# Kernel optimization log

Hardware: AMD Instinct MI355X
Metric: run time of the kernel (lower is better)

The kernel has to match this reference:

```python
import jax, jax.numpy as jnp
import numpy as np

B, L, E, H = 4, 2048, 512, 8


def setup_inputs() -> dict:
    key = jax.random.key(0)
    ks = jax.random.split(key, 12)
    s = 0.02
    inp = {
        "values": jax.random.normal(ks[0], (B, L, E), jnp.float32),
        "keys": jax.random.normal(ks[1], (B, L, E), jnp.float32),
        "queries": jax.random.normal(ks[2], (B, L, E), jnp.float32),
    }
    mask = jax.random.randint(ks[3], (B, L, H, H), 0, 2, jnp.int32)
    # guarantee at least one unmasked entry per softmax row to avoid NaN rows
    mask = mask.at[..., 0].set(1)
    inp["mask"] = mask
    # Linear(E, E*H) weights stored as (in, out); torch uses y = x @ W.T + b
    inp["Wv"] = jax.random.normal(ks[4], (E, E * H), jnp.float32) * s
    inp["bv"] = jnp.zeros((E * H,), jnp.float32)
    inp["Wk"] = jax.random.normal(ks[5], (E, E * H), jnp.float32) * s
    inp["bk"] = jnp.zeros((E * H,), jnp.float32)
    inp["Wq"] = jax.random.normal(ks[6], (E, E * H), jnp.float32) * s
    inp["bq"] = jnp.zeros((E * H,), jnp.float32)
    inp["Wo"] = jax.random.normal(ks[7], (E * H, E), jnp.float32) * s
    inp["bo"] = jnp.zeros((E,), jnp.float32)
    return inp


def reference(values, keys, queries, mask, Wv, bv, Wk, bk, Wq, bq, Wo, bo):
    b, l, e = queries.shape
    h = Wq.shape[1] // e

    def proj(x, W, bias):
        # (B,L,E) -> (B,L,H,E) -> transpose(1,2) -> (B,H,L,E)
        return (x @ W + bias).reshape(b, -1, h, e).transpose(0, 2, 1, 3)

    v = proj(values, Wv, bv)
    k = proj(keys, Wk, bk)
    q = proj(queries, Wq, bq)
    # Faithful to source: einsum labels applied to the TRANSPOSED (B,H,L,E)
    # tensors, so 'q'/'k' bind to the heads axis and 'h' binds to seq axis.
    # energy: (B, L, H, H) -- head-vs-head scores at each position.
    energy = jnp.einsum('nqhd,nkhd->nhqk', q, k)
    energy = jnp.where(mask == 0, -jnp.inf, energy)
    attn = jax.nn.softmax(energy / jnp.sqrt(jnp.float32(e)), axis=3)
    # out of einsum: (B, H, L, E); raw row-major reshape to (B, L, H*E)
    out = jnp.einsum('nhql,nlhd->nqhd', attn, v).reshape(b, -1, h * e)
    return out @ Wo + bo
```

## Files before the change

### kernel.cpp

```cpp
#include <hip/hip_runtime.h>
#include <stdint.h>

typedef __attribute__((ext_vector_type(4))) float f32x4;
typedef __attribute__((ext_vector_type(8))) __bf16 bf16x8;

__device__ __forceinline__ unsigned short f2bf(float f) {
  union { float f; uint32_t u; } v; v.f = f;
  uint32_t u = v.u;
  return (unsigned short)((u + 0x7FFFu + ((u >> 16) & 1u)) >> 16);
}
__device__ __forceinline__ float bflo(uint32_t u) {
  union { uint32_t u; float f; } v; v.u = u << 16; return v.f;
}
__device__ __forceinline__ float bfhi(uint32_t u) {
  union { uint32_t u; float f; } v; v.u = u & 0xffff0000u; return v.f;
}

__device__ __forceinline__ void async_copy16(void* lds, const void* g) {
  __builtin_amdgcn_global_load_lds(
      (const __attribute__((address_space(1))) void*)g,
      (__attribute__((address_space(3))) void*)lds,
      16, 0, 0);
}

__global__ void cvt3_f32_bf16(const float* __restrict__ in0,
                              const float* __restrict__ in1,
                              const float* __restrict__ in2,
                              uint32_t* __restrict__ out, int n) {
  const float* in = (blockIdx.y == 0) ? in0 : (blockIdx.y == 1) ? in1 : in2;
  uint32_t* o = out + (size_t)blockIdx.y * (n / 2);
  int i = blockIdx.x * blockDim.x + threadIdx.x;
  int idx = i * 8;
  if (idx >= n) return;
  float4 a = *(const float4*)(in + idx);
  float4 b = *(const float4*)(in + idx + 4);
  uint4 ov;
  ov.x = f2bf(a.x) | ((uint32_t)f2bf(a.y) << 16);
  ov.y = f2bf(a.z) | ((uint32_t)f2bf(a.w) << 16);
  ov.z = f2bf(b.x) | ((uint32_t)f2bf(b.y) << 16);
  ov.w = f2bf(b.z) | ((uint32_t)f2bf(b.w) << 16);
  *(uint4*)(o + i * 4) = ov;
}

__global__ void transpose3_to_bf16(const float* __restrict__ in0,
                                   const float* __restrict__ in1,
                                   const float* __restrict__ in2,
                                   unsigned short* __restrict__ out,
                                   int R, int C) {
  const float* in = (blockIdx.z == 0) ? in0 : (blockIdx.z == 1) ? in1 : in2;
  unsigned short* o = out + (size_t)blockIdx.z * ((size_t)R * C);
  __shared__ float tile[32][33];
  int c0 = blockIdx.x * 32, r0 = blockIdx.y * 32;
  int tx = threadIdx.x, ty = threadIdx.y;
  #pragma unroll
  for (int rr = 0; rr < 32; rr += 8)
    tile[ty + rr][tx] = in[(size_t)(r0 + ty + rr) * C + c0 + tx];
  __syncthreads();
  #pragma unroll
  for (int rr = 0; rr < 32; rr += 8)
    o[(size_t)(c0 + ty + rr) * R + r0 + tx] = f2bf(tile[tx][ty + rr]);
}

__global__ void transpose_to_bf16(const float* __restrict__ in,
                                  unsigned short* __restrict__ out,
                                  int R, int C) {
  __shared__ float tile[32][33];
  int c0 = blockIdx.x * 32, r0 = blockIdx.y * 32;
  int tx = threadIdx.x, ty = threadIdx.y;
  #pragma unroll
  for (int rr = 0; rr < 32; rr += 8)
    tile[ty + rr][tx] = in[(size_t)(r0 + ty + rr) * C + c0 + tx];
  __syncthreads();
  #pragma unroll
  for (int rr = 0; rr < 32; rr += 8)
    out[(size_t)(c0 + ty + rr) * R + r0 + tx] = f2bf(tile[tx][ty + rr]);
}

template <int NK, int NN, bool PARTIAL>
__global__ __launch_bounds__(512, 2) void gemm256(
    const unsigned short* __restrict__ A,
    const unsigned short* __restrict__ Bt,
    const float* __restrict__ bias,
    void* __restrict__ Cout,
    int Mt, int NtG, int KC, int Kfull) {
  constexpr int TT = NK * NN;
  static_assert(TT >= 4 && (TT % 2) == 0, "need even TT >= 4");
  __shared__ unsigned short lds[2 * 2 * 256 * 64];

  const int nwg = Mt * NtG * KC;
  const int cpx = nwg >> 3;
  const int bid = blockIdx.x;
  const int nb = (bid & 7) * cpx + (bid >> 3);
  const int kc = nb / (Mt * NtG);
  const int r2 = nb % (Mt * NtG);
  const int bm = r2 / NtG;
  const int ng = r2 % NtG;
  const int N = NtG * NN * 256;
  const size_t koff = (size_t)kc * (NK * 64);

  const int tid = threadIdx.x;
  const int wv = tid >> 6, ln = tid & 63;
  const int wm = wv >> 2, wn = wv & 3;

  f32x4 acc[8][4] = {};
  bf16x8 af[4][2];
  bf16x8 bfb[2][2];

  char* const lds0 = (char*)lds;
  char* const lds1 = (char*)lds + 65536;

  auto stage_A = [&](int h, int tau, char* dstbuf) {
    const int kt = tau % NK;
    #pragma unroll
    for (int r = 0; r < 2; ++r) {
      const int rb = r * 128 + h * 64 + wv * 8;
      const int row = rb + (ln >> 3);
      const int kcs = (ln & 7) ^ (row & 7);
      const unsigned short* g =
          A + (size_t)(bm * 256 + row) * Kfull + koff + kt * 64 + kcs * 8;
      async_copy16(dstbuf + rb * 128, g);
    }
  };
  auto stage_B = [&](int h, int tau, char* dstbuf) {
    const int kt = tau % NK;
    const int bnn = ng * NN + tau / NK;
    #pragma unroll
    for (int r = 0; r < 2; ++r) {
      const int s = r * 2 + (wv >> 2);
      const int rb = s * 64 + h * 32 + (wv & 3) * 8;
      const int row = rb + (ln >> 3);
      const int kcs = (ln & 7) ^ (row & 7);
      const unsigned short* g =
          Bt + (size_t)(bnn * 256 + row) * Kfull + koff + kt * 64 + kcs * 8;
      async_copy16(dstbuf + 32768 + rb * 128, g);
    }
  };
  auto load_af = [&](int mh, const char* buf) {
    #pragma unroll
    for (int f = 0; f < 4; ++f) {
      const int lr = wm * 128 + (mh * 4 + f) * 16 + (ln & 15);
      #pragma unroll
      for (int s = 0; s < 2; ++s) {
        const int kq = s * 4 + (ln >> 4);
        af[f][s] = *(const bf16x8*)(buf + lr * 128 + ((kq ^ (lr & 7)) * 16));
      }
    }
  };
  auto load_bf = [&](int nh, const char* buf) {
    #pragma unroll
    for (int gq = 0; gq < 2; ++gq) {
      const int lr = wn * 64 + (nh * 2 + gq) * 16 + (ln & 15);
      #pragma unroll
      for (int s = 0; s < 2; ++s) {
        const int kq = s * 4 + (ln >> 4);
        bfb[gq][s] =
            *(const bf16x8*)(buf + 32768 + lr * 128 + ((kq ^ (lr & 7)) * 16));
      }
    }
  };
  auto mfma_quad = [&](int mh, int nh) {
    __builtin_amdgcn_sched_barrier(0);
    __builtin_amdgcn_s_barrier();
    __builtin_amdgcn_sched_barrier(0);
    __builtin_amdgcn_s_setprio(1);
    #pragma unroll
    for (int f = 0; f < 4; ++f)
      #pragma unroll
      for (int gq = 0; gq < 2; ++gq)
        #pragma unroll
        for (int s = 0; s < 2; ++s)
          acc[mh * 4 + f][nh * 2 + gq] = __builtin_amdgcn_mfma_f32_16x16x32_bf16(
              bfb[gq][s], af[f][s], acc[mh * 4 + f][nh * 2 + gq], 0, 0, 0);
    __builtin_amdgcn_s_setprio(0);
    __builtin_amdgcn_sched_barrier(0);
  };
  auto epilogue = [&](int nt) {
    const int m0 = bm * 256 + wm * 128 + (ln & 15);
    const int n0 = (ng * NN + nt) * 256 + wn * 64 + ((ln >> 4) << 2);
    if (PARTIAL) {
      float* Cp = (float*)Cout + (size_t)kc * ((size_t)Mt * 256) * N;
      #pragma unroll
      for (int f = 0; f < 8; ++f) {
        const int row = m0 + f * 16;
        #pragma unroll
        for (int g = 0; g < 4; ++g)
          *(f32x4*)(Cp + (size_t)row * N + n0 + g * 16) = acc[f][g];
      }
    } else {
      unsigned short* C = (unsigned short*)Cout;
      #pragma unroll
      for (int f = 0; f < 8; ++f) {
        const int row = m0 + f * 16;
        #pragma unroll
        for (int g = 0; g < 4; ++g) {
          const int col = n0 + g * 16;
          float4 bv = *(const float4*)(bias + col);
          uint2 o;
          o.x = f2bf(acc[f][g][0] + bv.x) | ((uint32_t)f2bf(acc[f][g][1] + bv.y) << 16);
          o.y = f2bf(acc[f][g][2] + bv.z) | ((uint32_t)f2bf(acc[f][g][3] + bv.w) << 16);
          *(uint2*)(C + (size_t)row * N + col) = o;
        }
      }
    }
    #pragma unroll
    for (int f = 0; f < 8; ++f)
      #pragma unroll
      for (int g = 0; g < 4; ++g)
        acc[f][g] = (f32x4){0.f, 0.f, 0.f, 0.f};
  };

  auto tile_body = [&](int tau, char* buf, char* obuf) {
    load_af(0, buf); load_bf(0, buf);
    if (tau + 1 < TT) stage_B(0, tau + 1, obuf);
    mfma_quad(0, 0);
    __builtin_amdgcn_s_barrier();
    load_bf(1, buf);
    if (tau + 2 < TT) stage_A(0, tau + 2, buf);
    mfma_quad(0, 1);
    __builtin_amdgcn_s_barrier();
    load_af(1, buf);
    if (tau + 2 < TT) stage_B(1, tau + 2, buf);
    mfma_quad(1, 1);
    __builtin_amdgcn_s_barrier();
    load_bf(0, buf);
    if (tau + 2 < TT) stage_A(1, tau + 2, buf);
    mfma_quad(1, 0);
    if (tau + 2 < TT) {
      asm volatile("s_waitcnt vmcnt(6)" ::: "memory");
    } else if (tau + 1 < TT) {
      asm volatile("s_waitcnt vmcnt(0)" ::: "memory");
    }
    __builtin_amdgcn_sched_barrier(0);
    __builtin_amdgcn_s_barrier();
    if ((tau + 1) % NK == 0) epilogue(tau / NK);
  };

  stage_A(0, 0, lds0); stage_B(1, 0, lds0); stage_A(1, 0, lds0); stage_B(0, 0, lds0);
  stage_A(0, 1, lds1); stage_B(1, 1, lds1); stage_A(1, 1, lds1);
  asm volatile("s_waitcnt vmcnt(6)" ::: "memory");
  __builtin_amdgcn_sched_barrier(0);
  __builtin_amdgcn_s_barrier();

  for (int it = 0; it < TT / 2; ++it) {
    tile_body(2 * it,     lds0, lds1);
    tile_body(2 * it + 1, lds1, lds0);
  }
}

__global__ void reduce4_bias(const float* __restrict__ p,
                             const float* __restrict__ bo,
                             float* __restrict__ out) {
  const size_t S = (size_t)8192 * 512;
  size_t i = ((size_t)blockIdx.x * 256 + threadIdx.x) * 4;
  float4 a = *(const float4*)(p + i);
  float4 b = *(const float4*)(p + S + i);
  float4 c = *(const float4*)(p + 2 * S + i);
  float4 d = *(const float4*)(p + 3 * S + i);
  float4 bb = *(const float4*)(bo + (int)(i & 511));
  float4 o;
  o.x = a.x + b.x + c.x + d.x + bb.x;
  o.y = a.y + b.y + c.y + d.y + bb.y;
  o.z = a.z + b.z + c.z + d.z + bb.z;
  o.w = a.w + b.w + c.w + d.w + bb.w;
  *(float4*)(out + i) = o;
}

__global__ __launch_bounds__(256) void energy_mfma(
    const unsigned short* __restrict__ Q,
    const unsigned short* __restrict__ Kb,
    const int* __restrict__ mask,
    float* __restrict__ P) {
  const int wave = threadIdx.x >> 6, ln = threadIdx.x & 63;
  const int t2 = (blockIdx.x * 4 + wave) * 2;
  const int r16 = ln & 15;
  const int g = ln >> 4;
  const size_t rowoff = (size_t)(t2 + (r16 >> 3)) * 4096 + (r16 & 7) * 512 + g * 8;
  const unsigned short* qb = Q + rowoff;
  const unsigned short* kb = Kb + rowoff;

  f32x4 acc = {};
  #pragma unroll
  for (int s = 0; s < 16; ++s) {
    bf16x8 qf = *(const bf16x8*)(qb + s * 32);
    bf16x8 kf = *(const bf16x8*)(kb + s * 32);
    acc = __builtin_amdgcn_mfma_f32_16x16x32_bf16(qf, kf, acc, 0, 0, 0);
  }

  const int ct = r16 >> 3, j = r16 & 7;
  const bool valid = ((g >> 1) == ct);
  const int tok = t2 + ct;
  float pv[4];
  #pragma unroll
  for (int r = 0; r < 4; ++r) {
    const int i = (g & 1) * 4 + r;
    float e = acc[r] * 0.044194173824159216f;
    int mk = 1;
    if (valid) mk = mask[(size_t)tok * 64 + i * 8 + j];
    if (mk == 0) e = -1e30f;
    float m = e;
    m = fmaxf(m, __shfl_xor(m, 1, 64));
    m = fmaxf(m, __shfl_xor(m, 2, 64));
    m = fmaxf(m, __shfl_xor(m, 4, 64));
    float p = __expf(e - m);
    float sum = p;
    sum += __shfl_xor(sum, 1, 64);
    sum += __shfl_xor(sum, 2, 64);
    sum += __shfl_xor(sum, 4, 64);
    pv[r] = p / sum;
  }
  if (valid) {
    #pragma unroll
    for (int r = 0; r < 4; ++r) {
      const int i = (g & 1) * 4 + r;
      P[(size_t)tok * 64 + i * 8 + j] = pv[r];
    }
  }
}

__global__ __launch_bounds__(256) void pv_kernel(
    const float* __restrict__ P,
    const unsigned short* __restrict__ Vb,
    unsigned short* __restrict__ out2) {
  const int wave = threadIdx.x >> 6, lane = threadIdx.x & 63;
  const int t = blockIdx.x * 4 + wave;
  const unsigned short* Vr = Vb + (size_t)t * 4096;
  float att = P[(size_t)t * 64 + lane];

  uint4 v4[8];
  #pragma unroll
  for (int jj = 0; jj < 8; ++jj)
    v4[jj] = *(const uint4*)(Vr + jj * 512 + lane * 8);

  const int nb = t >> 11, l = t & 2047;
  const size_t tok_base = (size_t)nb * 8388608 + (size_t)(l >> 3) * 4096 +
                          (size_t)(l & 7) * 512 + lane * 8;
  #pragma unroll
  for (int hh = 0; hh < 8; ++hh) {
    float accv[8] = {0.f, 0.f, 0.f, 0.f, 0.f, 0.f, 0.f, 0.f};
    #pragma unroll
    for (int jj = 0; jj < 8; ++jj) {
      float a = __shfl(att, hh * 8 + jj, 64);
      accv[0] += a * bflo(v4[jj].x); accv[1] += a * bfhi(v4[jj].x);
      accv[2] += a * bflo(v4[jj].y); accv[3] += a * bfhi(v4[jj].y);
      accv[4] += a * bflo(v4[jj].z); accv[5] += a * bfhi(v4[jj].z);
      accv[6] += a * bflo(v4[jj].w); accv[7] += a * bfhi(v4[jj].w);
    }
    uint4 o;
    o.x = f2bf(accv[0]) | ((uint32_t)f2bf(accv[1]) << 16);
    o.y = f2bf(accv[2]) | ((uint32_t)f2bf(accv[3]) << 16);
    o.z = f2bf(accv[4]) | ((uint32_t)f2bf(accv[5]) << 16);
    o.w = f2bf(accv[6]) | ((uint32_t)f2bf(accv[7]) << 16);
    *(uint4*)(out2 + tok_base + (size_t)hh * 1048576) = o;
  }
}

extern "C" void kernel_launch(void* const* d_in, const int* in_sizes, int n_in,
                              void* d_out, int out_size, void* d_ws, size_t ws_size,
                              hipStream_t stream) {
  const float* values  = (const float*)d_in[0];
  const float* keys    = (const float*)d_in[1];
  const float* queries = (const float*)d_in[2];
  const int*   mask    = (const int*)d_in[3];
  const float* Wv = (const float*)d_in[4];
  const float* bv = (const float*)d_in[5];
  const float* Wk = (const float*)d_in[6];
  const float* bk = (const float*)d_in[7];
  const float* Wq = (const float*)d_in[8];
  const float* bq = (const float*)d_in[9];
  const float* Wo = (const float*)d_in[10];
  const float* bo = (const float*)d_in[11];

  unsigned short* xv  = (unsigned short*)d_ws;
  unsigned short* xk  = xv + 8192 * 512;
  unsigned short* xq  = xk + 8192 * 512;
  unsigned short* Wvt = xq + 8192 * 512;
  unsigned short* Wkt = Wvt + 4096 * 512;
  unsigned short* Wqt = Wkt + 4096 * 512;
  unsigned short* Wot = Wqt + 4096 * 512;
  float*          P   = (float*)(Wot + 4096 * 512);
  unsigned short* bufA = (unsigned short*)(P + 8192 * 64);
  unsigned short* bufB = bufA + (size_t)8192 * 4096;

  const int nx = 8192 * 512;
  cvt3_f32_bf16<<<dim3(nx / 8 / 256, 3), 256, 0, stream>>>(
      values, keys, queries, (uint32_t*)xv, nx);

  transpose3_to_bf16<<<dim3(4096 / 32, 512 / 32, 3), dim3(32, 8), 0, stream>>>(
      Wv, Wk, Wq, Wvt, 512, 4096);
  transpose_to_bf16<<<dim3(512 / 32, 4096 / 32), dim3(32, 8), 0, stream>>>(
      Wo, Wot, 4096, 512);

  gemm256<8, 2, false><<<256, 512, 0, stream>>>(xq, Wqt, bq, bufA, 32, 8, 1, 512);
  gemm256<8, 2, false><<<256, 512, 0, stream>>>(xk, Wkt, bk, bufB, 32, 8, 1, 512);

  energy_mfma<<<8192 / 8, 256, 0, stream>>>(bufA, bufB, mask, P);

  gemm256<8, 2, false><<<256, 512, 0, stream>>>(xv, Wvt, bv, bufA, 32, 8, 1, 512);

  pv_kernel<<<8192 / 4, 256, 0, stream>>>(P, bufA, bufB);

  gemm256<16, 1, true><<<256, 512, 0, stream>>>(bufB, Wot, nullptr, (float*)bufA,
                                                32, 2, 4, 4096);
  reduce4_bias<<<4096, 256, 0, stream>>>((float*)bufA, bo, (float*)d_out);
}
```

Measured before the change: 280.9 us.

## Restructure GEMM tile loop into two halves with all B fragments loaded once

```diff
diff --git a/kernel.cpp b/kernel.cpp
--- a/kernel.cpp
+++ b/kernel.cpp
@@ -104,7 +104,7 @@
 
   f32x4 acc[8][4] = {};
   bf16x8 af[4][2];
-  bf16x8 bfb[2][2];
+  bf16x8 bfb[4][2];
 
   char* const lds0 = (char*)lds;
   char* const lds1 = (char*)lds + 65536;
@@ -146,19 +146,19 @@
       }
     }
   };
-  auto load_bf = [&](int nh, const char* buf) {
-    #pragma unroll
-    for (int gq = 0; gq < 2; ++gq) {
-      const int lr = wn * 64 + (nh * 2 + gq) * 16 + (ln & 15);
+  auto load_bf_all = [&](const char* buf) {
+    #pragma unroll
+    for (int c = 0; c < 4; ++c) {
+      const int lr = wn * 64 + c * 16 + (ln & 15);
       #pragma unroll
       for (int s = 0; s < 2; ++s) {
         const int kq = s * 4 + (ln >> 4);
-        bfb[gq][s] =
+        bfb[c][s] =
             *(const bf16x8*)(buf + 32768 + lr * 128 + ((kq ^ (lr & 7)) * 16));
       }
     }
   };
-  auto mfma_quad = [&](int mh, int nh) {
+  auto mfma_half = [&](int mh) {
     __builtin_amdgcn_sched_barrier(0);
     __builtin_amdgcn_s_barrier();
     __builtin_amdgcn_sched_barrier(0);
@@ -166,11 +166,11 @@
     #pragma unroll
     for (int f = 0; f < 4; ++f)
       #pragma unroll
-      for (int gq = 0; gq < 2; ++gq)
+      for (int c = 0; c < 4; ++c)
         #pragma unroll
         for (int s = 0; s < 2; ++s)
-          acc[mh * 4 + f][nh * 2 + gq] = __builtin_amdgcn_mfma_f32_16x16x32_bf16(
-              bfb[gq][s], af[f][s], acc[mh * 4 + f][nh * 2 + gq], 0, 0, 0);
+          acc[mh * 4 + f][c] = __builtin_amdgcn_mfma_f32_16x16x32_bf16(
+              bfb[c][s], af[f][s], acc[mh * 4 + f][c], 0, 0, 0);
     __builtin_amdgcn_s_setprio(0);
     __builtin_amdgcn_sched_barrier(0);
   };
@@ -210,23 +210,16 @@
   };
 
   auto tile_body = [&](int tau, char* buf, char* obuf) {
-    load_af(0, buf); load_bf(0, buf);
-    if (tau + 1 < TT) stage_B(0, tau + 1, obuf);
-    mfma_quad(0, 0);
-    __builtin_amdgcn_s_barrier();
-    load_bf(1, buf);
-    if (tau + 2 < TT) stage_A(0, tau + 2, buf);
-    mfma_quad(0, 1);
+    load_af(0, buf);
+    load_bf_all(buf);
+    if (tau + 1 < TT) { stage_A(1, tau + 1, obuf); stage_B(1, tau + 1, obuf); }
+    mfma_half(0);
     __builtin_amdgcn_s_barrier();
     load_af(1, buf);
-    if (tau + 2 < TT) stage_B(1, tau + 2, buf);
-    mfma_quad(1, 1);
-    __builtin_amdgcn_s_barrier();
-    load_bf(0, buf);
-    if (tau + 2 < TT) stage_A(1, tau + 2, buf);
-    mfma_quad(1, 0);
+    if (tau + 2 < TT) { stage_A(0, tau + 2, buf); stage_B(0, tau + 2, buf); }
+    mfma_half(1);
     if (tau + 2 < TT) {
-      asm volatile("s_waitcnt vmcnt(6)" ::: "memory");
+      asm volatile("s_waitcnt vmcnt(4)" ::: "memory");
     } else if (tau + 1 < TT) {
       asm volatile("s_waitcnt vmcnt(0)" ::: "memory");
     }
@@ -235,9 +228,9 @@
     if ((tau + 1) % NK == 0) epilogue(tau / NK);
   };
 
-  stage_A(0, 0, lds0); stage_B(1, 0, lds0); stage_A(1, 0, lds0); stage_B(0, 0, lds0);
-  stage_A(0, 1, lds1); stage_B(1, 1, lds1); stage_A(1, 1, lds1);
-  asm volatile("s_waitcnt vmcnt(6)" ::: "memory");
+  stage_A(0, 0, lds0); stage_B(0, 0, lds0); stage_A(1, 0, lds0); stage_B(1, 0, lds0);
+  stage_A(0, 1, lds1); stage_B(0, 1, lds1);
+  asm volatile("s_waitcnt vmcnt(4)" ::: "memory");
   __builtin_amdgcn_sched_barrier(0);
   __builtin_amdgcn_s_barrier();
 
```

After: 322.9 us. 15.0% more time.

## Merge Q and K projection GEMMs into one launch and simplify the pipeline

Applied to the files above, without the earlier changes.

```diff
diff --git a/kernel.cpp b/kernel.cpp
--- a/kernel.cpp
+++ b/kernel.cpp
@@ -76,12 +76,16 @@
     out[(size_t)(c0 + ty + rr) * R + r0 + tx] = f2bf(tile[tx][ty + rr]);
 }
 
-template <int NK, int NN, bool PARTIAL>
+template <int NK, int NN, bool PARTIAL, bool DUAL>
 __global__ __launch_bounds__(512, 2) void gemm256(
     const unsigned short* __restrict__ A,
     const unsigned short* __restrict__ Bt,
     const float* __restrict__ bias,
     void* __restrict__ Cout,
+    const unsigned short* __restrict__ A2,
+    const unsigned short* __restrict__ Bt2,
+    const float* __restrict__ bias2,
+    void* __restrict__ Cout2,
     int Mt, int NtG, int KC, int Kfull) {
   constexpr int TT = NK * NN;
   static_assert(TT >= 4 && (TT % 2) == 0, "need even TT >= 4");
@@ -95,8 +99,15 @@
   const int r2 = nb % (Mt * NtG);
   const int bm = r2 / NtG;
   const int ng = r2 % NtG;
-  const int N = NtG * NN * 256;
+  const int mat = DUAL ? (ng >> 3) : 0;
+  const int ngm = DUAL ? (ng & 7) : ng;
+  const int N = (DUAL ? (NtG >> 1) : NtG) * NN * 256;
   const size_t koff = (size_t)kc * (NK * 64);
+
+  const unsigned short* Asrc = (DUAL && mat) ? A2 : A;
+  const unsigned short* Bsrc = (DUAL && mat) ? Bt2 : Bt;
+  const float* biasd = (DUAL && mat) ? bias2 : bias;
+  void* Cd = (DUAL && mat) ? Cout2 : Cout;
 
   const int tid = threadIdx.x;
   const int wv = tid >> 6, ln = tid & 63;
@@ -109,30 +120,18 @@
   char* const lds0 = (char*)lds;
   char* const lds1 = (char*)lds + 65536;
 
-  auto stage_A = [&](int h, int tau, char* dstbuf) {
-    const int kt = tau % NK;
-    #pragma unroll
-    for (int r = 0; r < 2; ++r) {
-      const int rb = r * 128 + h * 64 + wv * 8;
+  auto stage_tile = [&](int tt, char* dst) {
+    const int kt = tt % NK;
+    const int bnn = ngm * NN + tt / NK;
+    #pragma unroll
+    for (int i = 0; i < 4; ++i) {
+      const int rb = i * 64 + wv * 8;
       const int row = rb + (ln >> 3);
       const int kcs = (ln & 7) ^ (row & 7);
-      const unsigned short* g =
-          A + (size_t)(bm * 256 + row) * Kfull + koff + kt * 64 + kcs * 8;
-      async_copy16(dstbuf + rb * 128, g);
-    }
-  };
-  auto stage_B = [&](int h, int tau, char* dstbuf) {
-    const int kt = tau % NK;
-    const int bnn = ng * NN + tau / NK;
-    #pragma unroll
-    for (int r = 0; r < 2; ++r) {
-      const int s = r * 2 + (wv >> 2);
-      const int rb = s * 64 + h * 32 + (wv & 3) * 8;
-      const int row = rb + (ln >> 3);
-      const int kcs = (ln & 7) ^ (row & 7);
-      const unsigned short* g =
-          Bt + (size_t)(bnn * 256 + row) * Kfull + koff + kt * 64 + kcs * 8;
-      async_copy16(dstbuf + 32768 + rb * 128, g);
+      async_copy16(dst + rb * 128,
+                   Asrc + (size_t)(bm * 256 + row) * Kfull + koff + kt * 64 + kcs * 8);
+      async_copy16(dst + 32768 + rb * 128,
+                   Bsrc + (size_t)(bnn * 256 + row) * Kfull + koff + kt * 64 + kcs * 8);
     }
   };
   auto load_af = [&](int mh, const char* buf) {
@@ -159,9 +158,6 @@
     }
   };
   auto mfma_quad = [&](int mh, int nh) {
-    __builtin_amdgcn_sched_barrier(0);
-    __builtin_amdgcn_s_barrier();
-    __builtin_amdgcn_sched_barrier(0);
     __builtin_amdgcn_s_setprio(1);
     #pragma unroll
     for (int f = 0; f < 4; ++f)
@@ -172,13 +168,12 @@
           acc[mh * 4 + f][nh * 2 + gq] = __builtin_amdgcn_mfma_f32_16x16x32_bf16(
               bfb[gq][s], af[f][s], acc[mh * 4 + f][nh * 2 + gq], 0, 0, 0);
     __builtin_amdgcn_s_setprio(0);
-    __builtin_amdgcn_sched_barrier(0);
   };
   auto epilogue = [&](int nt) {
     const int m0 = bm * 256 + wm * 128 + (ln & 15);
-    const int n0 = (ng * NN + nt) * 256 + wn * 64 + ((ln >> 4) << 2);
+    const int n0 = (ngm * NN + nt) * 256 + wn * 64 + ((ln >> 4) << 2);
     if (PARTIAL) {
-      float* Cp = (float*)Cout + (size_t)kc * ((size_t)Mt * 256) * N;
+      float* Cp = (float*)Cd + (size_t)kc * ((size_t)Mt * 256) * N;
       #pragma unroll
       for (int f = 0; f < 8; ++f) {
         const int row = m0 + f * 16;
@@ -187,14 +182,14 @@
           *(f32x4*)(Cp + (size_t)row * N + n0 + g * 16) = acc[f][g];
       }
     } else {
-      unsigned short* C = (unsigned short*)Cout;
+      unsigned short* C = (unsigned short*)Cd;
       #pragma unroll
       for (int f = 0; f < 8; ++f) {
         const int row = m0 + f * 16;
         #pragma unroll
         for (int g = 0; g < 4; ++g) {
           const int col = n0 + g * 16;
-          float4 bv = *(const float4*)(bias + col);
+          float4 bv = *(const float4*)(biasd + col);
           uint2 o;
           o.x = f2bf(acc[f][g][0] + bv.x) | ((uint32_t)f2bf(acc[f][g][1] + bv.y) << 16);
           o.y = f2bf(acc[f][g][2] + bv.z) | ((uint32_t)f2bf(acc[f][g][3] + bv.w) << 16);
@@ -209,35 +204,28 @@
         acc[f][g] = (f32x4){0.f, 0.f, 0.f, 0.f};
   };
 
-  auto tile_body = [&](int tau, char* buf, char* obuf) {
+  auto tile_body = [&](int tau, const char* buf, char* obuf) {
+    if (tau + 1 < TT) stage_tile(tau + 1, obuf);
     load_af(0, buf); load_bf(0, buf);
-    if (tau + 1 < TT) stage_B(0, tau + 1, obuf);
     mfma_quad(0, 0);
-    __builtin_amdgcn_s_barrier();
+    __builtin_amdgcn_sched_barrier(0);
     load_bf(1, buf);
-    if (tau + 2 < TT) stage_A(0, tau + 2, buf);
     mfma_quad(0, 1);
-    __builtin_amdgcn_s_barrier();
+    __builtin_amdgcn_sched_barrier(0);
     load_af(1, buf);
-    if (tau + 2 < TT) stage_B(1, tau + 2, buf);
     mfma_quad(1, 1);
-    __builtin_amdgcn_s_barrier();
+    __builtin_amdgcn_sched_barrier(0);
     load_bf(0, buf);
-    if (tau + 2 < TT) stage_A(1, tau + 2, buf);
     mfma_quad(1, 0);
-    if (tau + 2 < TT) {
-      asm volatile("s_waitcnt vmcnt(6)" ::: "memory");
-    } else if (tau + 1 < TT) {
+    __builtin_amdgcn_sched_barrier(0);
+    if (tau + 1 < TT)
       asm volatile("s_waitcnt vmcnt(0)" ::: "memory");
-    }
-    __builtin_amdgcn_sched_barrier(0);
     __builtin_amdgcn_s_barrier();
     if ((tau + 1) % NK == 0) epilogue(tau / NK);
   };
 
-  stage_A(0, 0, lds0); stage_B(1, 0, lds0); stage_A(1, 0, lds0); stage_B(0, 0, lds0);
-  stage_A(0, 1, lds1); stage_B(1, 1, lds1); stage_A(1, 1, lds1);
-  asm volatile("s_waitcnt vmcnt(6)" ::: "memory");
+  stage_tile(0, lds0);
+  asm volatile("s_waitcnt vmcnt(0)" ::: "memory");
   __builtin_amdgcn_sched_barrier(0);
   __builtin_amdgcn_s_barrier();
 
@@ -390,16 +378,18 @@
   transpose_to_bf16<<<dim3(512 / 32, 4096 / 32), dim3(32, 8), 0, stream>>>(
       Wo, Wot, 4096, 512);
 
-  gemm256<8, 2, false><<<256, 512, 0, stream>>>(xq, Wqt, bq, bufA, 32, 8, 1, 512);
-  gemm256<8, 2, false><<<256, 512, 0, stream>>>(xk, Wkt, bk, bufB, 32, 8, 1, 512);
+  gemm256<8, 2, false, true><<<512, 512, 0, stream>>>(
+      xq, Wqt, bq, bufA, xk, Wkt, bk, bufB, 32, 16, 1, 512);
 
   energy_mfma<<<8192 / 8, 256, 0, stream>>>(bufA, bufB, mask, P);
 
-  gemm256<8, 2, false><<<256, 512, 0, stream>>>(xv, Wvt, bv, bufA, 32, 8, 1, 512);
+  gemm256<8, 2, false, false><<<256, 512, 0, stream>>>(
+      xv, Wvt, bv, bufA, nullptr, nullptr, nullptr, nullptr, 32, 8, 1, 512);
 
   pv_kernel<<<8192 / 4, 256, 0, stream>>>(P, bufA, bufB);
 
-  gemm256<16, 1, true><<<256, 512, 0, stream>>>(bufB, Wot, nullptr, (float*)bufA,
-                                                32, 2, 4, 4096);
+  gemm256<16, 1, true, false><<<256, 512, 0, stream>>>(
+      bufB, Wot, nullptr, (float*)bufA, nullptr, nullptr, nullptr, nullptr,
+      32, 2, 4, 4096);
   reduce4_bias<<<4096, 256, 0, stream>>>((float*)bufA, bo, (float*)d_out);
 }
```

Measured after the change: 264.3 us. 5.9% less time.
